# Optimization experiments

Hardware: AMD Instinct MI355X
Metric: run time of the kernel (lower is better)

The kernel has to match this reference:

```python
import jax, jax.numpy as jnp
import numpy as np

B, N, D, T = 32, 512, 128, 8
NEG_SLOPE = 0.2
MASK_VAL = -1e10


def _xavier(key, shape, gain=1.0):
    fan_in, fan_out = shape[0], int(np.prod(shape[1:]))
    limit = gain * np.sqrt(6.0 / (fan_in + fan_out))
    return jax.random.uniform(key, shape, jnp.float32, -limit, limit)


def setup_inputs() -> dict:
    key = jax.random.key(0)
    ks = jax.random.split(key, 8)
    atom_embeddings = jax.random.normal(ks[0], (B, N, D), dtype=jnp.float32)
    # bond types in [-1, T-1]; -1 = no bond (masked)
    edges = jax.random.randint(ks[1], (B, N, N), 0, T + 1, dtype=jnp.int64) - 1
    Qw = _xavier(ks[2], (D, D))
    Kw = _xavier(ks[3], (D, D))
    Vw = _xavier(ks[4], (D, D))
    Pw = _xavier(ks[5], (D, D))
    Qb = jnp.zeros((D,), jnp.float32)
    Kb = jnp.zeros((D,), jnp.float32)
    Vb = jnp.zeros((D,), jnp.float32)
    Pb = jnp.zeros((D,), jnp.float32)
    a = _xavier(ks[6], (D, D, T), gain=1.414)
    return {"atom_embeddings": atom_embeddings, "edges": edges,
            "Qw": Qw, "Qb": Qb, "Kw": Kw, "Kb": Kb, "Vw": Vw, "Vb": Vb,
            "a": a, "Pw": Pw, "Pb": Pb}


def reference(atom_embeddings, edges, Qw, Qb, Kw, Kb, Vw, Vb, a, Pw, Pb):
    # torch Linear: x @ W.T + b
    src = atom_embeddings @ Qw.T + Qb            # (B,N,D)
    dst = atom_embeddings @ Kw.T + Kb            # (B,N,D)
    val = atom_embeddings @ Vw.T + Vb            # (B,N,D)

    # bilinear edge-type scores: s[b,n,m,t] = src[b,n,:] @ a[:,:,t] @ dst[b,m,:]
    ts = jnp.einsum('bnd,det->bnet', src, a)     # (B,N,D,T)
    scores = jnp.einsum('bnet,bme->bnmt', ts, dst)  # (B,N,N,T)

    # gather the slice for each edge's bond type (clamp -1 -> 0 like torch)
    idx = jnp.clip(edges, 0, None)[..., None]    # (B,N,N,1)
    att = jnp.take_along_axis(scores, idx, axis=-1)[..., 0]  # (B,N,N)
    att = jnp.where(edges == -1, MASK_VAL, att)
    att = jnp.where(att >= 0, att, NEG_SLOPE * att)  # leaky_relu
    att = jax.nn.softmax(att, axis=-1)           # (B,N,N)

    out = att @ val                              # (B,N,D)
    return out @ Pw.T + Pb
```

## Files before the change

kernel.cpp:

```cpp
#include <hip/hip_runtime.h>
#include <stdint.h>


typedef short bf16x8 __attribute__((ext_vector_type(8)));
typedef float f32x4 __attribute__((ext_vector_type(4)));
typedef unsigned short u16;
typedef unsigned int u32;
typedef unsigned long long u64;

__device__ __forceinline__ u16 f2bf(float x) {
    union { float f; u32 u; } v; v.f = x;
    u32 r = v.u + 0x7FFFu + ((v.u >> 16) & 1u);
    return (u16)(r >> 16);
}
__device__ __forceinline__ float bf2f(u16 h) {
    union { u32 u; float f; } v; v.u = ((u32)h) << 16; return v.f;
}
__device__ __forceinline__ void split_hl(float x, u16& h, u16& l) {
    h = f2bf(x);
    l = f2bf(x - bf2f(h));
}
__device__ __forceinline__ void split4(float4 x, u64& hq, u64& lq) {
    u16 h0, l0, h1, l1, h2, l2, h3, l3;
    split_hl(x.x, h0, l0); split_hl(x.y, h1, l1);
    split_hl(x.z, h2, l2); split_hl(x.w, h3, l3);
    hq = (u64)h0 | ((u64)h1 << 16) | ((u64)h2 << 32) | ((u64)h3 << 48);
    lq = (u64)l0 | ((u64)l1 << 16) | ((u64)l2 << 32) | ((u64)l3 << 48);
}
__device__ __forceinline__ f32x4 mfma16(bf16x8 a, bf16x8 b, f32x4 c) {
    return __builtin_amdgcn_mfma_f32_16x16x32_bf16(a, b, c, 0, 0, 0);
}

__global__ void prep_kernel(const float* __restrict__ Qw, const float* __restrict__ Qb,
                            const float* __restrict__ Kw, const float* __restrict__ Kb,
                            const float* __restrict__ Vw, const float* __restrict__ Vb,
                            const float* __restrict__ Aa, const float* __restrict__ Pw,
                            u16* __restrict__ WH, u16* __restrict__ WL,
                            float* __restrict__ bcat) {
    int gid = blockIdx.x * 256 + threadIdx.x;
    if (gid >= 1280 * 128) return;
    int j = gid >> 7, d = gid & 127;
    float v, bias = 0.f;
    if (j < 128) { v = Kw[j * 128 + d]; bias = Kb[j]; }
    else if (j < 256) {
        int jj = j - 128;
        float s = 0.f, bs = 0.f;
        for (int k = 0; k < 128; k++) {
            float p = Pw[jj * 128 + k];
            s += p * Vw[k * 128 + d];
            bs += p * Vb[k];
        }
        v = s; bias = bs;
    } else {
        int r = j - 256, t = r >> 7, jj = r & 127;
        float s = 0.f, bs = 0.f;
        for (int e = 0; e < 128; e++) {
            float av = Aa[(e * 128 + jj) * 8 + t];
            s += Qw[e * 128 + d] * av;
            bs += Qb[e] * av;
        }
        v = s; bias = bs;
    }
    u16 h, l; split_hl(v, h, l);
    WH[gid] = h; WL[gid] = l;
    if (d == 0) bcat[j] = bias;
}

__global__ void detect_kernel(const int* __restrict__ E, int* __restrict__ flag) {
    __shared__ int bad;
    if (threadIdx.x == 0) bad = 0;
    __syncthreads();
    int w0 = E[2 * threadIdx.x + 1];
    int w1 = E[2 * (threadIdx.x + 256) + 1];
    if (!(w0 == 0 || w0 == -1) || !(w1 == 0 || w1 == -1)) atomicOr(&bad, 1);
    __syncthreads();
    if (threadIdx.x == 0) *flag = (bad ? 0 : 1);
}

__global__ void econv_kernel(const void* __restrict__ E, const int* __restrict__ flag,
                             signed char* __restrict__ E8) {
    int i = (blockIdx.x * 256 + threadIdx.x) * 4;
    char4 o;
    if (*flag) {
        const long long* p = (const long long*)E;
        o.x = (signed char)p[i]; o.y = (signed char)p[i + 1];
        o.z = (signed char)p[i + 2]; o.w = (signed char)p[i + 3];
    } else {
        const int* p = (const int*)E;
        o.x = (signed char)p[i]; o.y = (signed char)p[i + 1];
        o.z = (signed char)p[i + 2]; o.w = (signed char)p[i + 3];
    }
    *(char4*)(E8 + i) = o;
}

__launch_bounds__(256, 2)
__global__ void gemm1_kernel(const float* __restrict__ X,
                             const u16* __restrict__ WH, const u16* __restrict__ WL,
                             const float* __restrict__ bcat,
                             float* __restrict__ C,
                             u16* __restrict__ VTH, u16* __restrict__ VTL) {
    const int id = blockIdx.x;
    const int xcd = id & 7, q5 = id >> 3;
    const int g0 = (xcd * 32 + (q5 >> 1)) * 64;
    const int jbase = (q5 & 1) * 10;
    __shared__ u16 WB[2][2][64 * 128];
    const int tid = threadIdx.x;
    const int wid = tid >> 6, lane = tid & 63;
    const int gblk = (wid >> 1) * 32, jblk = (wid & 1) * 32;
    const int lr = lane & 15, lg = lane >> 4;

    {
        const float4* Xv = (const float4*)(X + (size_t)g0 * 128);
        #pragma unroll
        for (int i = 0; i < 8; i++) {
            int idx = tid + i * 256;
            float4 x = Xv[idx];
            int row = idx >> 5, c4 = idx & 31;
            int boff = (row * 256 + c4 * 8) ^ ((row & 7) << 4);
            u64 hq, lq; split4(x, hq, lq);
            *(u64*)((char*)WB[1][0] + boff) = hq;
            *(u64*)((char*)WB[1][1] + boff) = lq;
        }
    }
    uint4 nh[4], nl[4];
    {
        const uint4* bh = (const uint4*)(WH + (size_t)(jbase + 0) * 64 * 128);
        const uint4* bl = (const uint4*)(WL + (size_t)(jbase + 0) * 64 * 128);
        #pragma unroll
        for (int i = 0; i < 4; i++) { nh[i] = bh[tid + i * 256]; nl[i] = bl[tid + i * 256]; }
    }
    __syncthreads();
    bf16x8 afh[4][2], afl[4][2];
    #pragma unroll
    for (int ks = 0; ks < 4; ks++) {
        const int kb2 = (ks * 32 + lg * 8) * 2;
        #pragma unroll
        for (int r = 0; r < 2; r++) {
            int row = gblk + r * 16 + lr;
            int boff = (row * 256 + kb2) ^ ((row & 7) << 4);
            afh[ks][r] = *(const bf16x8*)((const char*)WB[1][0] + boff);
            afl[ks][r] = *(const bf16x8*)((const char*)WB[1][1] + boff);
        }
    }
    #pragma unroll
    for (int i = 0; i < 4; i++) {
        int idx = tid + i * 256;
        int row = idx >> 4, ch = idx & 15;
        int boff = (row * 256 + ch * 16) ^ ((row & 7) << 4);
        *(uint4*)((char*)WB[0][0] + boff) = nh[i];
        *(uint4*)((char*)WB[0][1] + boff) = nl[i];
    }

    for (int jt = 0; jt < 10; jt++) {
        __syncthreads();
        if (jt < 9) {
            const uint4* bh = (const uint4*)(WH + (size_t)(jbase + jt + 1) * 64 * 128);
            const uint4* bl = (const uint4*)(WL + (size_t)(jbase + jt + 1) * 64 * 128);
            #pragma unroll
            for (int i = 0; i < 4; i++) { nh[i] = bh[tid + i * 256]; nl[i] = bl[tid + i * 256]; }
        }
        const int cur = jt & 1;
        const int j0 = (jbase + jt) * 64;
        const bool valTile = (j0 >= 128 && j0 < 256);
        f32x4 acc[2][2] = {};
        if (valTile) {
            #pragma unroll
            for (int ks = 0; ks < 4; ks++) {
                const int kb2 = (ks * 32 + lg * 8) * 2;
                bf16x8 bfh[2], bfl[2];
                #pragma unroll
                for (int c = 0; c < 2; c++) {
                    int row = jblk + c * 16 + lr;
                    int boff = (row * 256 + kb2) ^ ((row & 7) << 4);
                    bfh[c] = *(const bf16x8*)((const char*)WB[cur][0] + boff);
                    bfl[c] = *(const bf16x8*)((const char*)WB[cur][1] + boff);
                }
                #pragma unroll
                for (int r = 0; r < 2; r++)
                #pragma unroll
                for (int c = 0; c < 2; c++) {
                    acc[r][c] = mfma16(afh[ks][r], bfh[c], acc[r][c]);
                    acc[r][c] = mfma16(afh[ks][r], bfl[c], acc[r][c]);
                    acc[r][c] = mfma16(afl[ks][r], bfh[c], acc[r][c]);
                }
            }
            const int b = g0 >> 9;
            #pragma unroll
            for (int r = 0; r < 2; r++)
            #pragma unroll
            for (int c = 0; c < 2; c++) {
                int j = j0 + jblk + c * 16 + lr;
                float bias = bcat[j];
                int d = j - 128;
                int n = (g0 & 511) + gblk + r * 16 + 4 * lg;
                u64 hq, lq;
                float4 v = {acc[r][c][0] + bias, acc[r][c][1] + bias,
                            acc[r][c][2] + bias, acc[r][c][3] + bias};
                split4(v, hq, lq);
                size_t off = ((size_t)(b * 128 + d)) * 512 + n;
                *(u64*)(VTH + off) = hq;
                *(u64*)(VTL + off) = lq;
            }
        } else {
            #pragma unroll
            for (int ks = 0; ks < 4; ks++) {
                const int kb2 = (ks * 32 + lg * 8) * 2;
                bf16x8 bfh[2], bfl[2];
                #pragma unroll
                for (int c = 0; c < 2; c++) {
                    int row = jblk + c * 16 + lr;
                    int boff = (row * 256 + kb2) ^ ((row & 7) << 4);
                    bfh[c] = *(const bf16x8*)((const char*)WB[cur][0] + boff);
                    bfl[c] = *(const bf16x8*)((const char*)WB[cur][1] + boff);
                }
                #pragma unroll
                for (int c = 0; c < 2; c++)
                #pragma unroll
                for (int r = 0; r < 2; r++) {
                    acc[c][r] = mfma16(bfh[c], afh[ks][r], acc[c][r]);
                    acc[c][r] = mfma16(bfh[c], afl[ks][r], acc[c][r]);
                    acc[c][r] = mfma16(bfl[c], afh[ks][r], acc[c][r]);
                }
            }
            #pragma unroll
            for (int c = 0; c < 2; c++)
            #pragma unroll
            for (int r = 0; r < 2; r++) {
                int j = j0 + jblk + c * 16 + 4 * lg;
                int g = g0 + gblk + r * 16 + lr;
                float4 bias4 = *(const float4*)(bcat + j);
                float4 v = {acc[c][r][0] + bias4.x, acc[c][r][1] + bias4.y,
                            acc[c][r][2] + bias4.z, acc[c][r][3] + bias4.w};
                *(float4*)(C + (size_t)g * 1280 + j) = v;
            }
        }
        if (jt < 9) {
            #pragma unroll
            for (int i = 0; i < 4; i++) {
                int idx = tid + i * 256;
                int row = idx >> 4, ch = idx & 15;
                int boff = (row * 256 + ch * 16) ^ ((row & 7) << 4);
                *(uint4*)((char*)WB[cur ^ 1][0] + boff) = nh[i];
                *(uint4*)((char*)WB[cur ^ 1][1] + boff) = nl[i];
            }
        }
    }
}

__launch_bounds__(512, 2)
__global__ void scores_kernel(const float* __restrict__ C,
                              const signed char* __restrict__ E8,
                              float* __restrict__ att) {
    const int id = blockIdx.x;
    const int xcd = id & 7, j = id >> 3;
    const int m0 = (j & 3) * 128;
    const int pair = xcd * 32 + (j >> 2);
    const int n0 = (pair & 7) * 64, b = pair >> 3;
    __shared__ u16 BH[128 * 128], BL[128 * 128];
    __shared__ u16 AH[2][64 * 128], AL[2][64 * 128];
    const int tid = threadIdx.x;
    const int wid = tid >> 6, lane = tid & 63;
    const int wr = (wid >> 2) * 32, wc = (wid & 3) * 32;
    const int lr = lane & 15, lg = lane >> 4;

    #pragma unroll
    for (int i = 0; i < 8; i++) {
        int idx = tid + i * 512;
        int row = idx >> 5, c4 = idx & 31;
        float4 x = *(const float4*)(C + (size_t)(b * 512 + m0 + row) * 1280 + c4 * 4);
        u64 hq, lq; split4(x, hq, lq);
        int boff = (row * 256 + c4 * 8) ^ ((row & 7) << 4);
        *(u64*)((char*)BH + boff) = hq;
        *(u64*)((char*)BL + boff) = lq;
    }
    int ed[2][2][4];
    #pragma unroll
    for (int r = 0; r < 2; r++)
    #pragma unroll
    for (int c = 0; c < 2; c++)
    #pragma unroll
    for (int q = 0; q < 4; q++) {
        int n = n0 + wr + r * 16 + 4 * lg + q;
        int m = m0 + wc + c * 16 + lr;
        ed[r][c][q] = E8[((size_t)b * 512 + n) * 512 + m];
    }
    {
        #pragma unroll
        for (int i = 0; i < 4; i++) {
            int idx = tid + i * 512;
            int row = idx >> 5, c4 = idx & 31;
            float4 x = *(const float4*)(C + (size_t)(b * 512 + n0 + row) * 1280 + 256 + c4 * 4);
            u64 hq, lq; split4(x, hq, lq);
            int boff = (row * 256 + c4 * 8) ^ ((row & 7) << 4);
            *(u64*)((char*)AH[0] + boff) = hq;
            *(u64*)((char*)AL[0] + boff) = lq;
        }
    }
    __syncthreads();
    bf16x8 bfh[4][2], bfl[4][2];
    #pragma unroll
    for (int ks = 0; ks < 4; ks++) {
        const int kb2 = (ks * 32 + lg * 8) * 2;
        #pragma unroll
        for (int c = 0; c < 2; c++) {
            int row = wc + c * 16 + lr;
            int boff = (row * 256 + kb2) ^ ((row & 7) << 4);
            bfh[ks][c] = *(const bf16x8*)((const char*)BH + boff);
            bfl[ks][c] = *(const bf16x8*)((const char*)BL + boff);
        }
    }
    float sel[2][2][4];
    #pragma unroll
    for (int r = 0; r < 2; r++)
    #pragma unroll
    for (int c = 0; c < 2; c++)
    #pragma unroll
    for (int q = 0; q < 4; q++) sel[r][c][q] = 0.f;

    for (int t = 0; t < 8; t++) {
        const int cur = t & 1;
        float4 nx[4];
        if (t < 7) {
            #pragma unroll
            for (int i = 0; i < 4; i++) {
                int idx = tid + i * 512;
                int row = idx >> 5, c4 = idx & 31;
                nx[i] = *(const float4*)(C + (size_t)(b * 512 + n0 + row) * 1280
                                           + 256 + (t + 1) * 128 + c4 * 4);
            }
        }
        f32x4 acc[2][2] = {};
        __builtin_amdgcn_s_setprio(1);
        #pragma unroll
        for (int ks = 0; ks < 4; ks++) {
            const int kb2 = (ks * 32 + lg * 8) * 2;
            bf16x8 afh[2], afl[2];
            #pragma unroll
            for (int r = 0; r < 2; r++) {
                int row = wr + r * 16 + lr;
                int boff = (row * 256 + kb2) ^ ((row & 7) << 4);
                afh[r] = *(const bf16x8*)((const char*)AH[cur] + boff);
                afl[r] = *(const bf16x8*)((const char*)AL[cur] + boff);
            }
            #pragma unroll
            for (int r = 0; r < 2; r++)
            #pragma unroll
            for (int c = 0; c < 2; c++) {
                acc[r][c] = mfma16(afh[r], bfh[ks][c], acc[r][c]);
                acc[r][c] = mfma16(afh[r], bfl[ks][c], acc[r][c]);
                acc[r][c] = mfma16(afl[r], bfh[ks][c], acc[r][c]);
            }
        }
        __builtin_amdgcn_s_setprio(0);
        #pragma unroll
        for (int r = 0; r < 2; r++)
        #pragma unroll
        for (int c = 0; c < 2; c++)
        #pragma unroll
        for (int q = 0; q < 4; q++) {
            int ec = ed[r][c][q] < 0 ? 0 : ed[r][c][q];
            sel[r][c][q] = (ec == t) ? acc[r][c][q] : sel[r][c][q];
        }
        if (t < 7) {
            #pragma unroll
            for (int i = 0; i < 4; i++) {
                int idx = tid + i * 512;
                int row = idx >> 5, c4 = idx & 31;
                u64 hq, lq; split4(nx[i], hq, lq);
                int boff = (row * 256 + c4 * 8) ^ ((row & 7) << 4);
                *(u64*)((char*)AH[cur ^ 1] + boff) = hq;
                *(u64*)((char*)AL[cur ^ 1] + boff) = lq;
            }
        }
        __syncthreads();
    }
    #pragma unroll
    for (int r = 0; r < 2; r++)
    #pragma unroll
    for (int c = 0; c < 2; c++)
    #pragma unroll
    for (int q = 0; q < 4; q++) {
        float v = (ed[r][c][q] == -1) ? -1e10f : sel[r][c][q];
        v = (v >= 0.f) ? v : 0.2f * v;
        size_t n = n0 + wr + r * 16 + 4 * lg + q;
        size_t m = m0 + wc + c * 16 + lr;
        att[((size_t)b * 512 + n) * 512 + m] = v;
    }
}

__launch_bounds__(256, 2)
__global__ void out_kernel(const float* __restrict__ att,
                           const u16* __restrict__ VTH, const u16* __restrict__ VTL,
                           const float* __restrict__ Pb, float* __restrict__ out) {
    const int id = blockIdx.x;
    const int xcd = id & 7, j = id >> 3;
    const int b = xcd * 4 + (j >> 4);
    const int n0 = (j & 15) * 32;
    __shared__ u16 PH[32 * 64], PL[32 * 64];
    __shared__ u16 VH[128 * 64], VL[128 * 64];
    const int tid = threadIdx.x;
    const int row = tid >> 3, c8 = tid & 7;
    float4 av0[8], av1[8];
    const float4* rp = (const float4*)(att + ((size_t)b * 512 + n0 + row) * 512);
    #pragma unroll
    for (int mc = 0; mc < 8; mc++) {
        av0[mc] = rp[mc * 16 + c8 * 2];
        av1[mc] = rp[mc * 16 + c8 * 2 + 1];
    }
    float mx = -1e30f;
    #pragma unroll
    for (int mc = 0; mc < 8; mc++) {
        mx = fmaxf(mx, fmaxf(fmaxf(fmaxf(av0[mc].x, av0[mc].y), fmaxf(av0[mc].z, av0[mc].w)),
                             fmaxf(fmaxf(av1[mc].x, av1[mc].y), fmaxf(av1[mc].z, av1[mc].w))));
    }
    #pragma unroll
    for (int o = 1; o < 8; o <<= 1) mx = fmaxf(mx, __shfl_xor(mx, o, 64));
    float s = 0.f;
    #pragma unroll
    for (int mc = 0; mc < 8; mc++) {
        av0[mc].x = expf(av0[mc].x - mx); av0[mc].y = expf(av0[mc].y - mx);
        av0[mc].z = expf(av0[mc].z - mx); av0[mc].w = expf(av0[mc].w - mx);
        av1[mc].x = expf(av1[mc].x - mx); av1[mc].y = expf(av1[mc].y - mx);
        av1[mc].z = expf(av1[mc].z - mx); av1[mc].w = expf(av1[mc].w - mx);
        s += av0[mc].x + av0[mc].y + av0[mc].z + av0[mc].w
           + av1[mc].x + av1[mc].y + av1[mc].z + av1[mc].w;
    }
    #pragma unroll
    for (int o = 1; o < 8; o <<= 1) s += __shfl_xor(s, o, 64);
    const float inv = 1.0f / s;
    const int wid = tid >> 6, lane = tid & 63;
    const int lr = lane & 15, lg = lane >> 4;
    const int wc = wid * 32;
    f32x4 acc[2][2] = {};
    for (int mc = 0; mc < 8; mc++) {
        {
            float4 p0 = {av0[mc].x * inv, av0[mc].y * inv, av0[mc].z * inv, av0[mc].w * inv};
            float4 p1 = {av1[mc].x * inv, av1[mc].y * inv, av1[mc].z * inv, av1[mc].w * inv};
            u64 h0, l0, h1, l1;
            split4(p0, h0, l0); split4(p1, h1, l1);
            int boff = (row * 128 + c8 * 16) ^ ((row & 7) << 4);
            *(u64*)((char*)PH + boff) = h0;
            *(u64*)((char*)PH + boff + 8) = h1;
            *(u64*)((char*)PL + boff) = l0;
            *(u64*)((char*)PL + boff + 8) = l1;
        }
        #pragma unroll
        for (int i = 0; i < 4; i++) {
            int idx = tid + i * 256;
            int vrow = idx >> 3, ch = idx & 7;
            size_t src = ((size_t)(b * 128 + vrow)) * 512 + mc * 64;
            int boff = (vrow * 128 + ch * 16) ^ ((vrow & 7) << 4);
            *(uint4*)((char*)VH + boff) = ((const uint4*)(VTH + src))[ch];
            *(uint4*)((char*)VL + boff) = ((const uint4*)(VTL + src))[ch];
        }
        __syncthreads();
        #pragma unroll
        for (int ks = 0; ks < 2; ks++) {
            const int kb2 = (ks * 32 + lg * 8) * 2;
            bf16x8 ah[2], al[2];
            #pragma unroll
            for (int r = 0; r < 2; r++) {
                int prow = r * 16 + lr;
                int boff = (prow * 128 + kb2) ^ ((prow & 7) << 4);
                ah[r] = *(const bf16x8*)((const char*)PH + boff);
                al[r] = *(const bf16x8*)((const char*)PL + boff);
            }
            #pragma unroll
            for (int c = 0; c < 2; c++) {
                int vrow = wc + c * 16 + lr;
                int boff = (vrow * 128 + kb2) ^ ((vrow & 7) << 4);
                bf16x8 bh = *(const bf16x8*)((const char*)VH + boff);
                bf16x8 bl = *(const bf16x8*)((const char*)VL + boff);
                #pragma unroll
                for (int r = 0; r < 2; r++) {
                    acc[r][c] = mfma16(ah[r], bh, acc[r][c]);
                    acc[r][c] = mfma16(ah[r], bl, acc[r][c]);
                    acc[r][c] = mfma16(al[r], bh, acc[r][c]);
                }
            }
        }
        __syncthreads();
    }
    #pragma unroll
    for (int r = 0; r < 2; r++)
    #pragma unroll
    for (int c = 0; c < 2; c++)
    #pragma unroll
    for (int q = 0; q < 4; q++) {
        int n = n0 + r * 16 + 4 * lg + q;
        int d = wc + c * 16 + lr;
        out[((size_t)b * 512 + n) * 128 + d] = acc[r][c][q] + Pb[d];
    }
}

extern "C" void kernel_launch(void* const* d_in, const int* in_sizes, int n_in,
                              void* d_out, int out_size, void* d_ws, size_t ws_size,
                              hipStream_t stream) {
    (void)in_sizes; (void)n_in; (void)out_size; (void)ws_size;
    const float* X  = (const float*)d_in[0];
    const void*  E  = d_in[1];
    const float* Qw = (const float*)d_in[2];
    const float* Qb = (const float*)d_in[3];
    const float* Kw = (const float*)d_in[4];
    const float* Kb = (const float*)d_in[5];
    const float* Vw = (const float*)d_in[6];
    const float* Vb = (const float*)d_in[7];
    const float* Aa = (const float*)d_in[8];
    const float* Pw = (const float*)d_in[9];
    const float* Pb = (const float*)d_in[10];
    float* out = (float*)d_out;

    char* ws = (char*)d_ws;
    size_t cur = 0;
    auto alloc = [&](size_t bytes) -> char* {
        char* p = ws + cur;
        cur += (bytes + 255) & ~(size_t)255;
        return p;
    };
    int*   flag = (int*)  alloc(4);
    u16*   WH   = (u16*)  alloc((size_t)1280 * 128 * 2);
    u16*   WL   = (u16*)  alloc((size_t)1280 * 128 * 2);
    float* bcat = (float*)alloc(1280 * 4);
    float* C    = (float*)alloc((size_t)16384 * 1280 * 4);
    u16*   VTH  = (u16*)  alloc((size_t)32 * 128 * 512 * 2);
    u16*   VTL  = (u16*)  alloc((size_t)32 * 128 * 512 * 2);
    float* att  = (float*)alloc((size_t)32 * 512 * 512 * 4);
    signed char* E8 = (signed char*)alloc((size_t)32 * 512 * 512);

    prep_kernel<<<640, 256, 0, stream>>>(Qw, Qb, Kw, Kb, Vw, Vb, Aa, Pw, WH, WL, bcat);
    detect_kernel<<<1, 256, 0, stream>>>((const int*)E, flag);
    econv_kernel<<<8192, 256, 0, stream>>>(E, flag, E8);
    gemm1_kernel<<<512, 256, 0, stream>>>(X, WH, WL, bcat, C, VTH, VTL);
    scores_kernel<<<1024, 512, 0, stream>>>(C, E8, att);
    out_kernel<<<512, 256, 0, stream>>>(att, VTH, VTL, Pb, out);
}
```

Before: 264.3 us.

## Drop edge conversion pass, read edges directly, and stream fragment-layout weights from global

Removes the separate econv kernel that narrowed the edges tensor to int8; the scores kernel now reads the original int64/int32 edges directly, guided by the detected flag. The prep kernel writes the combined weights in an MFMA-fragment-ready layout so gemm1 loads B fragments straight from global/L2 instead of staging them through double-buffered shared memory. It also loads and splits the X fragments directly into registers. gemm1 now uses a 4-way j split over 1024 blocks with a higher occupancy hint. This trades a full pass over the edges tensor and the LDS staging and barriers for wider scattered edge reads in scores and more global weight traffic.

```diff
diff --git a/kernel.cpp b/kernel.cpp
--- a/kernel.cpp
+++ b/kernel.cpp
@@ -27,6 +27,15 @@
     hq = (u64)h0 | ((u64)h1 << 16) | ((u64)h2 << 32) | ((u64)h3 << 48);
     lq = (u64)l0 | ((u64)l1 << 16) | ((u64)l2 << 32) | ((u64)l3 << 48);
 }
+__device__ __forceinline__ void split8(float4 a, float4 b, bf16x8& h8, bf16x8& l8) {
+    u16 hh[8], ll[8];
+    split_hl(a.x, hh[0], ll[0]); split_hl(a.y, hh[1], ll[1]);
+    split_hl(a.z, hh[2], ll[2]); split_hl(a.w, hh[3], ll[3]);
+    split_hl(b.x, hh[4], ll[4]); split_hl(b.y, hh[5], ll[5]);
+    split_hl(b.z, hh[6], ll[6]); split_hl(b.w, hh[7], ll[7]);
+    #pragma unroll
+    for (int i = 0; i < 8; i++) { h8[i] = (short)hh[i]; l8[i] = (short)ll[i]; }
+}
 __device__ __forceinline__ f32x4 mfma16(bf16x8 a, bf16x8 b, f32x4 c) {
     return __builtin_amdgcn_mfma_f32_16x16x32_bf16(a, b, c, 0, 0, 0);
 }
@@ -35,7 +44,7 @@
                             const float* __restrict__ Kw, const float* __restrict__ Kb,
                             const float* __restrict__ Vw, const float* __restrict__ Vb,
                             const float* __restrict__ Aa, const float* __restrict__ Pw,
-                            u16* __restrict__ WH, u16* __restrict__ WL,
+                            u16* __restrict__ WFH, u16* __restrict__ WFL,
                             float* __restrict__ bcat) {
     int gid = blockIdx.x * 256 + threadIdx.x;
     if (gid >= 1280 * 128) return;
@@ -62,7 +71,8 @@
         v = s; bias = bs;
     }
     u16 h, l; split_hl(v, h, l);
-    WH[gid] = h; WL[gid] = l;
+    size_t idx = ((size_t)((j >> 4) * 16 + (d >> 3)) * 16 + (j & 15)) * 8 + (d & 7);
+    WFH[idx] = h; WFL[idx] = l;
     if (d == 0) bcat[j] = bias;
 }
 
@@ -77,103 +87,48 @@
     if (threadIdx.x == 0) *flag = (bad ? 0 : 1);
 }
 
-__global__ void econv_kernel(const void* __restrict__ E, const int* __restrict__ flag,
-                             signed char* __restrict__ E8) {
-    int i = (blockIdx.x * 256 + threadIdx.x) * 4;
-    char4 o;
-    if (*flag) {
-        const long long* p = (const long long*)E;
-        o.x = (signed char)p[i]; o.y = (signed char)p[i + 1];
-        o.z = (signed char)p[i + 2]; o.w = (signed char)p[i + 3];
-    } else {
-        const int* p = (const int*)E;
-        o.x = (signed char)p[i]; o.y = (signed char)p[i + 1];
-        o.z = (signed char)p[i + 2]; o.w = (signed char)p[i + 3];
-    }
-    *(char4*)(E8 + i) = o;
-}
-
-__launch_bounds__(256, 2)
+__launch_bounds__(256, 3)
 __global__ void gemm1_kernel(const float* __restrict__ X,
-                             const u16* __restrict__ WH, const u16* __restrict__ WL,
+                             const u16* __restrict__ WFH, const u16* __restrict__ WFL,
                              const float* __restrict__ bcat,
                              float* __restrict__ C,
                              u16* __restrict__ VTH, u16* __restrict__ VTL) {
     const int id = blockIdx.x;
-    const int xcd = id & 7, q5 = id >> 3;
-    const int g0 = (xcd * 32 + (q5 >> 1)) * 64;
-    const int jbase = (q5 & 1) * 10;
-    __shared__ u16 WB[2][2][64 * 128];
+    const int xcd = id & 7, q = id >> 3;
+    const int g0 = (xcd * 32 + (q >> 2)) * 64;
+    const int jsplit = q & 3;
     const int tid = threadIdx.x;
     const int wid = tid >> 6, lane = tid & 63;
     const int gblk = (wid >> 1) * 32, jblk = (wid & 1) * 32;
     const int lr = lane & 15, lg = lane >> 4;
 
-    {
-        const float4* Xv = (const float4*)(X + (size_t)g0 * 128);
-        #pragma unroll
-        for (int i = 0; i < 8; i++) {
-            int idx = tid + i * 256;
-            float4 x = Xv[idx];
-            int row = idx >> 5, c4 = idx & 31;
-            int boff = (row * 256 + c4 * 8) ^ ((row & 7) << 4);
-            u64 hq, lq; split4(x, hq, lq);
-            *(u64*)((char*)WB[1][0] + boff) = hq;
-            *(u64*)((char*)WB[1][1] + boff) = lq;
-        }
-    }
-    uint4 nh[4], nl[4];
-    {
-        const uint4* bh = (const uint4*)(WH + (size_t)(jbase + 0) * 64 * 128);
-        const uint4* bl = (const uint4*)(WL + (size_t)(jbase + 0) * 64 * 128);
-        #pragma unroll
-        for (int i = 0; i < 4; i++) { nh[i] = bh[tid + i * 256]; nl[i] = bl[tid + i * 256]; }
-    }
-    __syncthreads();
     bf16x8 afh[4][2], afl[4][2];
     #pragma unroll
-    for (int ks = 0; ks < 4; ks++) {
-        const int kb2 = (ks * 32 + lg * 8) * 2;
-        #pragma unroll
-        for (int r = 0; r < 2; r++) {
-            int row = gblk + r * 16 + lr;
-            int boff = (row * 256 + kb2) ^ ((row & 7) << 4);
-            afh[ks][r] = *(const bf16x8*)((const char*)WB[1][0] + boff);
-            afl[ks][r] = *(const bf16x8*)((const char*)WB[1][1] + boff);
-        }
-    }
-    #pragma unroll
-    for (int i = 0; i < 4; i++) {
-        int idx = tid + i * 256;
-        int row = idx >> 4, ch = idx & 15;
-        int boff = (row * 256 + ch * 16) ^ ((row & 7) << 4);
-        *(uint4*)((char*)WB[0][0] + boff) = nh[i];
-        *(uint4*)((char*)WB[0][1] + boff) = nl[i];
-    }
-
-    for (int jt = 0; jt < 10; jt++) {
-        __syncthreads();
-        if (jt < 9) {
-            const uint4* bh = (const uint4*)(WH + (size_t)(jbase + jt + 1) * 64 * 128);
-            const uint4* bl = (const uint4*)(WL + (size_t)(jbase + jt + 1) * 64 * 128);
-            #pragma unroll
-            for (int i = 0; i < 4; i++) { nh[i] = bh[tid + i * 256]; nl[i] = bl[tid + i * 256]; }
-        }
-        const int cur = jt & 1;
-        const int j0 = (jbase + jt) * 64;
-        const bool valTile = (j0 >= 128 && j0 < 256);
+    for (int ks = 0; ks < 4; ks++)
+    #pragma unroll
+    for (int r = 0; r < 2; r++) {
+        const float* p = X + (size_t)(g0 + gblk + r * 16 + lr) * 128 + ks * 32 + lg * 8;
+        float4 a = *(const float4*)p;
+        float4 b = *(const float4*)(p + 4);
+        split8(a, b, afh[ks][r], afl[ks][r]);
+    }
+
+    #pragma unroll
+    for (int jt5 = 0; jt5 < 5; jt5++) {
+        const int jt = jsplit * 5 + jt5;
+        const int j0 = jt * 64;
+        const bool valTile = (jt == 2 || jt == 3);
+        const int jgbase = (j0 + jblk) >> 4;
         f32x4 acc[2][2] = {};
         if (valTile) {
             #pragma unroll
             for (int ks = 0; ks < 4; ks++) {
-                const int kb2 = (ks * 32 + lg * 8) * 2;
                 bf16x8 bfh[2], bfl[2];
                 #pragma unroll
                 for (int c = 0; c < 2; c++) {
-                    int row = jblk + c * 16 + lr;
-                    int boff = (row * 256 + kb2) ^ ((row & 7) << 4);
-                    bfh[c] = *(const bf16x8*)((const char*)WB[cur][0] + boff);
-                    bfl[c] = *(const bf16x8*)((const char*)WB[cur][1] + boff);
+                    size_t eo = ((size_t)((jgbase + c) * 16 + ks * 4 + lg) * 16 + lr) * 8;
+                    bfh[c] = *(const bf16x8*)(WFH + eo);
+                    bfl[c] = *(const bf16x8*)(WFL + eo);
                 }
                 #pragma unroll
                 for (int r = 0; r < 2; r++)
@@ -193,10 +148,9 @@
                 float bias = bcat[j];
                 int d = j - 128;
                 int n = (g0 & 511) + gblk + r * 16 + 4 * lg;
-                u64 hq, lq;
                 float4 v = {acc[r][c][0] + bias, acc[r][c][1] + bias,
                             acc[r][c][2] + bias, acc[r][c][3] + bias};
-                split4(v, hq, lq);
+                u64 hq, lq; split4(v, hq, lq);
                 size_t off = ((size_t)(b * 128 + d)) * 512 + n;
                 *(u64*)(VTH + off) = hq;
                 *(u64*)(VTL + off) = lq;
@@ -204,14 +158,12 @@
         } else {
             #pragma unroll
             for (int ks = 0; ks < 4; ks++) {
-                const int kb2 = (ks * 32 + lg * 8) * 2;
                 bf16x8 bfh[2], bfl[2];
                 #pragma unroll
                 for (int c = 0; c < 2; c++) {
-                    int row = jblk + c * 16 + lr;
-                    int boff = (row * 256 + kb2) ^ ((row & 7) << 4);
-                    bfh[c] = *(const bf16x8*)((const char*)WB[cur][0] + boff);
-                    bfl[c] = *(const bf16x8*)((const char*)WB[cur][1] + boff);
+                    size_t eo = ((size_t)((jgbase + c) * 16 + ks * 4 + lg) * 16 + lr) * 8;
+                    bfh[c] = *(const bf16x8*)(WFH + eo);
+                    bfl[c] = *(const bf16x8*)(WFL + eo);
                 }
                 #pragma unroll
                 for (int c = 0; c < 2; c++)
@@ -234,22 +186,12 @@
                 *(float4*)(C + (size_t)g * 1280 + j) = v;
             }
         }
-        if (jt < 9) {
-            #pragma unroll
-            for (int i = 0; i < 4; i++) {
-                int idx = tid + i * 256;
-                int row = idx >> 4, ch = idx & 15;
-                int boff = (row * 256 + ch * 16) ^ ((row & 7) << 4);
-                *(uint4*)((char*)WB[cur ^ 1][0] + boff) = nh[i];
-                *(uint4*)((char*)WB[cur ^ 1][1] + boff) = nl[i];
-            }
-        }
     }
 }
 
 __launch_bounds__(512, 2)
 __global__ void scores_kernel(const float* __restrict__ C,
-                              const signed char* __restrict__ E8,
+                              const void* __restrict__ Eptr, const int* __restrict__ flag,
                               float* __restrict__ att) {
     const int id = blockIdx.x;
     const int xcd = id & 7, j = id >> 3;
@@ -262,6 +204,7 @@
     const int wid = tid >> 6, lane = tid & 63;
     const int wr = (wid >> 2) * 32, wc = (wid & 3) * 32;
     const int lr = lane & 15, lg = lane >> 4;
+    const bool e64 = (*flag != 0);
 
     #pragma unroll
     for (int i = 0; i < 8; i++) {
@@ -280,9 +223,10 @@
     for (int c = 0; c < 2; c++)
     #pragma unroll
     for (int q = 0; q < 4; q++) {
-        int n = n0 + wr + r * 16 + 4 * lg + q;
-        int m = m0 + wc + c * 16 + lr;
-        ed[r][c][q] = E8[((size_t)b * 512 + n) * 512 + m];
+        size_t n = n0 + wr + r * 16 + 4 * lg + q;
+        size_t m = m0 + wc + c * 16 + lr;
+        size_t idx = ((size_t)b * 512 + n) * 512 + m;
+        ed[r][c][q] = e64 ? (int)((const long long*)Eptr)[idx] : ((const int*)Eptr)[idx];
     }
     {
         #pragma unroll
@@ -518,19 +462,17 @@
         return p;
     };
     int*   flag = (int*)  alloc(4);
-    u16*   WH   = (u16*)  alloc((size_t)1280 * 128 * 2);
-    u16*   WL   = (u16*)  alloc((size_t)1280 * 128 * 2);
+    u16*   WFH  = (u16*)  alloc((size_t)1280 * 128 * 2);
+    u16*   WFL  = (u16*)  alloc((size_t)1280 * 128 * 2);
     float* bcat = (float*)alloc(1280 * 4);
     float* C    = (float*)alloc((size_t)16384 * 1280 * 4);
     u16*   VTH  = (u16*)  alloc((size_t)32 * 128 * 512 * 2);
     u16*   VTL  = (u16*)  alloc((size_t)32 * 128 * 512 * 2);
     float* att  = (float*)alloc((size_t)32 * 512 * 512 * 4);
-    signed char* E8 = (signed char*)alloc((size_t)32 * 512 * 512);
-
-    prep_kernel<<<640, 256, 0, stream>>>(Qw, Qb, Kw, Kb, Vw, Vb, Aa, Pw, WH, WL, bcat);
+
+    prep_kernel<<<640, 256, 0, stream>>>(Qw, Qb, Kw, Kb, Vw, Vb, Aa, Pw, WFH, WFL, bcat);
     detect_kernel<<<1, 256, 0, stream>>>((const int*)E, flag);
-    econv_kernel<<<8192, 256, 0, stream>>>(E, flag, E8);
-    gemm1_kernel<<<512, 256, 0, stream>>>(X, WH, WL, bcat, C, VTH, VTL);
-    scores_kernel<<<1024, 512, 0, stream>>>(C, E8, att);
+    gemm1_kernel<<<1024, 256, 0, stream>>>(X, WFH, WFL, bcat, C, VTH, VTL);
+    scores_kernel<<<1024, 512, 0, stream>>>(C, E, flag, att);
     out_kernel<<<512, 256, 0, stream>>>(att, VTH, VTL, Pb, out);
 }
```

After: 221.3 us. -16.3%, faster.
